# Optimization experiments

Hardware: AMD Instinct MI355X
Metric: run time of the kernel (lower is better)

The kernel has to match this reference:

```python
import jax, jax.numpy as jnp
import numpy as np

N_NODES = 100000


def _gcn_conv(x, src, dst, W, b):
    # symmetric normalization D^{-1/2} (A+I) D^{-1/2}, self loops already in src/dst
    deg = jax.ops.segment_sum(jnp.ones_like(src, dtype=x.dtype), dst, num_segments=N_NODES)
    dinv = jnp.where(deg > 0, jax.lax.rsqrt(jnp.maximum(deg, 1e-12)), 0.0)
    norm = dinv[src] * dinv[dst]                      # [E+N]
    h = x @ W                                          # [N, out] dense GEMM first (fewer features to move)
    msg = h[src] * norm[:, None]                       # gather + scale, [E+N, out]
    out = jax.ops.segment_sum(msg, dst, num_segments=N_NODES)
    return out + b


def setup_inputs() -> dict:
    key = jax.random.key(0)
    k_x, k_e, k_w1, k_w2 = jax.random.split(key, 4)
    in_f, hid, n_cls = 512, 128, 32
    E = 1600000
    x = jax.random.normal(k_x, (N_NODES, in_f), dtype=jnp.float32)
    edge_index = jax.random.randint(k_e, (2, E), 0, N_NODES, dtype=jnp.int32)
    # Glorot-ish init for weights
    W1 = jax.random.normal(k_w1, (in_f, hid), dtype=jnp.float32) * (1.0 / np.sqrt(in_f))
    b1 = jnp.zeros((hid,), dtype=jnp.float32)
    W2 = jax.random.normal(k_w2, (hid, n_cls), dtype=jnp.float32) * (1.0 / np.sqrt(hid))
    b2 = jnp.zeros((n_cls,), dtype=jnp.float32)
    return {"x": x, "edge_index": edge_index, "W1": W1, "b1": b1, "W2": W2, "b2": b2}


def reference(x, edge_index, W1, b1, W2, b2):
    loops = jnp.arange(N_NODES, dtype=edge_index.dtype)
    src = jnp.concatenate([edge_index[0], loops])
    dst = jnp.concatenate([edge_index[1], loops])
    h = _gcn_conv(x, src, dst, W1, b1)
    h = jax.nn.relu(h)
    # dropout in eval mode (identity) for deterministic reference
    out = _gcn_conv(h, src, dst, W2, b2)
    return out
```

## Files before the change

kernel.cpp:

```cpp
#include <hip/hip_runtime.h>
#include <hip/hip_bf16.h>
#include <cstddef>


#define IN_F 512
#define HID 128
#define NCLS 32

typedef __attribute__((ext_vector_type(8))) short bf16x8;
typedef __attribute__((ext_vector_type(4))) float f32x4;

__device__ __forceinline__ unsigned short f2bf(float f) {
    union { float f; unsigned u; } v; v.f = f;
    unsigned r = v.u + 0x7fff + ((v.u >> 16) & 1);
    return (unsigned short)(r >> 16);
}
__device__ __forceinline__ float bf2f(unsigned short h) {
    union { unsigned u; float f; } v; v.u = ((unsigned)h) << 16;
    return v.f;
}
__device__ __forceinline__ float lo16(unsigned u) { return bf2f((unsigned short)(u & 0xffff)); }
__device__ __forceinline__ float hi16(unsigned u) { return bf2f((unsigned short)(u >> 16)); }
__device__ __forceinline__ unsigned cvt_pk_bf16(float a, float b) {
    unsigned r;
    asm("v_cvt_pk_bf16_f32 %0, %1, %2" : "=v"(r) : "v"(a), "v"(b));
    return r;
}
__device__ __forceinline__ bf16x8 pk8(float4 lo, float4 hi) {
    union { uint4 u; bf16x8 v; } r;
    r.u.x = cvt_pk_bf16(lo.x, lo.y);
    r.u.y = cvt_pk_bf16(lo.z, lo.w);
    r.u.z = cvt_pk_bf16(hi.x, hi.y);
    r.u.w = cvt_pk_bf16(hi.z, hi.w);
    return r.v;
}

__global__ void k_histprep(const int* __restrict__ dst, int* __restrict__ deg,
                           int* __restrict__ rank, int E,
                           const float* __restrict__ W1, unsigned short* __restrict__ W1T,
                           const float* __restrict__ W2, unsigned short* __restrict__ W2T, int PB) {
    int b = blockIdx.x;
    if (b < PB) {
        int i = b * 256 + threadIdx.x;
        if (i < HID * IN_F) {
            int n = i >> 9, k = i & 511;
            W1T[(size_t)n * IN_F + k] = f2bf(W1[(size_t)k * HID + n]);
        } else {
            int j = i - HID * IN_F;
            int c = j >> 7, k = j & 127;
            W2T[(size_t)c * HID + k] = f2bf(W2[(size_t)k * NCLS + c]);
        }
    } else {
        int e = (b - PB) * 256 + threadIdx.x;
        if (e < E) rank[e] = atomicAdd(&deg[dst[e]], 1);
    }
}

__global__ __launch_bounds__(256) void k_scan1(const int* __restrict__ deg, int* __restrict__ rs,
                                               int* __restrict__ bsum, int n) {
    __shared__ int sd[256];
    int base = blockIdx.x * 2048 + threadIdx.x * 8;
    int v[8];
    int t = 0;
#pragma unroll
    for (int i = 0; i < 8; ++i) {
        int x = (base + i < n) ? ((deg[base + i] + 7) & ~7) : 0;
        v[i] = t;
        t += x;
    }
    sd[threadIdx.x] = t;
    __syncthreads();
    for (int off = 1; off < 256; off <<= 1) {
        int x = 0;
        if ((int)threadIdx.x >= off) x = sd[threadIdx.x - off];
        __syncthreads();
        if ((int)threadIdx.x >= off) sd[threadIdx.x] += x;
        __syncthreads();
    }
    int texcl = sd[threadIdx.x] - t;
#pragma unroll
    for (int i = 0; i < 8; ++i)
        if (base + i < n) rs[base + i] = texcl + v[i];
    if (threadIdx.x == 255) bsum[blockIdx.x] = sd[255];
}

__global__ __launch_bounds__(256) void k_scan3(int* __restrict__ rs, const int* __restrict__ bsum,
                                               const int* __restrict__ deg, int* __restrict__ csr,
                                               float* __restrict__ dinv,
                                               unsigned* __restrict__ hsu, unsigned* __restrict__ h2su,
                                               int n, int nb) {
    __shared__ int sb[256];
    __shared__ int se[256];
    int t = threadIdx.x;
    int val = (t < nb) ? bsum[t] : 0;
    sb[t] = val;
    __syncthreads();
    for (int off = 1; off < 256; off <<= 1) {
        int x = 0;
        if (t >= off) x = sb[t - off];
        __syncthreads();
        sb[t] += x;
        __syncthreads();
    }
    se[t] = sb[t] - val;
    __syncthreads();
    int i = blockIdx.x * 256 + t;
    if (i < n) {
        int d = deg[i];
        dinv[i] = rsqrtf((float)d + 1.0f);
        int r = rs[i] + se[i >> 11];
        rs[i] = r;
        int pc = (d + 7) & ~7;
        for (int j = d; j < pc; ++j) csr[r + j] = n;
    }
    if (blockIdx.x == 0) {
        if (t < 64) hsu[(size_t)n * 64 + t] = 0u;
        if (t < 16) h2su[(size_t)n * 16 + t] = 0u;
    }
}

#define SCHUNK 1024
__global__ __launch_bounds__(256) void k_fused(const float* __restrict__ A,
                                               const unsigned short* __restrict__ BT,
                                               const float* __restrict__ dinv,
                                               unsigned short* __restrict__ C, int M,
                                               const int* __restrict__ src, const int* __restrict__ dst,
                                               const int* __restrict__ rank, const int* __restrict__ rs,
                                               int* __restrict__ csr, int E) {
    const int bid = blockIdx.x;
    const int tid = threadIdx.x;
    if (bid & 1) {
        int base = (bid >> 1) * SCHUNK + tid;
        int d[4], s[4], rk[4];
        bool val[4];
#pragma unroll
        for (int j = 0; j < 4; ++j) {
            int e = base + j * 256;
            val[j] = e < E;
            if (val[j]) { d[j] = dst[e]; s[j] = src[e]; rk[j] = rank[e]; }
        }
#pragma unroll
        for (int j = 0; j < 4; ++j)
            if (val[j]) csr[rs[d[j]] + rk[j]] = s[j];
        return;
    }
    const int wave = tid >> 6;
    const int lane = tid & 63;
    const int l16 = lane & 15;
    const int q = lane >> 4;
    const int rowBase = (bid >> 1) * 64;
    const int arow = rowBase + wave * 16 + l16;
    const bool aval = arow < M;
    const float* aptr = A + (size_t)arow * IN_F + q * 8;
    const unsigned short* bptr = BT + (size_t)l16 * IN_F + q * 8;

    f32x4 acc[8];
#pragma unroll
    for (int nt = 0; nt < 8; ++nt) acc[nt] = (f32x4){0.f, 0.f, 0.f, 0.f};

    float4 a0, a1;
    bf16x8 bfr[8];
    auto ld = [&](int k0, float4& x0, float4& x1, bf16x8* bv) {
        if (aval) {
            x0 = *(const float4*)(aptr + k0);
            x1 = *(const float4*)(aptr + k0 + 4);
        } else {
            x0 = make_float4(0.f, 0.f, 0.f, 0.f);
            x1 = x0;
        }
#pragma unroll
        for (int nt = 0; nt < 8; ++nt)
            bv[nt] = *(const bf16x8*)(bptr + (size_t)nt * 16 * IN_F + k0);
    };

    ld(0, a0, a1, bfr);
    for (int t = 0; t < 16; ++t) {
        float4 na0, na1;
        bf16x8 nb[8];
        if (t < 15) ld((t + 1) * 32, na0, na1, nb);
        bf16x8 a_frag = pk8(a0, a1);
#pragma unroll
        for (int nt = 0; nt < 8; ++nt)
            acc[nt] = __builtin_amdgcn_mfma_f32_16x16x32_bf16(a_frag, bfr[nt], acc[nt], 0, 0, 0);
        a0 = na0; a1 = na1;
#pragma unroll
        for (int nt = 0; nt < 8; ++nt) bfr[nt] = nb[nt];
    }

#pragma unroll
    for (int r = 0; r < 4; ++r) {
        int row = rowBase + wave * 16 + q * 4 + r;
        if (row < M) {
            float sc = dinv[row];
#pragma unroll
            for (int nt = 0; nt < 8; ++nt)
                C[(size_t)row * HID + nt * 16 + l16] = f2bf(acc[nt][r] * sc);
        }
    }
}

__global__ __launch_bounds__(256) void k_agg1mm(const unsigned short* __restrict__ hs,
                                                const int* __restrict__ csr,
                                                const int* __restrict__ rs, const int* __restrict__ cnt,
                                                const float* __restrict__ dinv, const float* __restrict__ b1,
                                                const unsigned short* __restrict__ W2T,
                                                unsigned short* __restrict__ h2s, int N) {
    __shared__ unsigned h1s[16 * 68];
    const int tid = threadIdx.x;
    const int wave = tid >> 6;
    const int lane = tid & 63;
    const int base = blockIdx.x * 16;
    const unsigned* hrow = (const unsigned*)hs;
    float2 bb = ((const float2*)b1)[lane];
#pragma unroll
    for (int r = 0; r < 4; ++r) {
        int slot = wave * 4 + r;
        int v = base + slot;
        float ox = 0.f, oy = 0.f;
        if (v < N) {
            float dv = dinv[v];
            unsigned u = hrow[(size_t)v * 64 + lane];
            float ax = lo16(u), ay = hi16(u);
            int start = rs[v];
            int pc = (cnt[v] + 7) & ~7;
            for (int i = 0; i < pc; i += 8) {
                int s[8];
                unsigned uu[8];
#pragma unroll
                for (int j = 0; j < 8; ++j) s[j] = csr[start + i + j];
#pragma unroll
                for (int j = 0; j < 8; ++j) uu[j] = hrow[(size_t)s[j] * 64 + lane];
#pragma unroll
                for (int j = 0; j < 8; ++j) { ax += lo16(uu[j]); ay += hi16(uu[j]); }
            }
            ox = fmaxf(dv * ax + bb.x, 0.f);
            oy = fmaxf(dv * ay + bb.y, 0.f);
        }
        h1s[slot * 68 + lane] = cvt_pk_bf16(ox, oy);
    }
    __syncthreads();
    if (wave < 2) {
        const int l16 = lane & 15;
        const int q = lane >> 4;
        f32x4 acc = (f32x4){0.f, 0.f, 0.f, 0.f};
        const unsigned short* h1b = (const unsigned short*)h1s;
#pragma unroll
        for (int ks = 0; ks < 4; ++ks) {
            bf16x8 af = *(const bf16x8*)(h1b + l16 * 136 + ks * 32 + q * 8);
            bf16x8 bf_ = *(const bf16x8*)(W2T + (size_t)(wave * 16 + l16) * HID + ks * 32 + q * 8);
            acc = __builtin_amdgcn_mfma_f32_16x16x32_bf16(af, bf_, acc, 0, 0, 0);
        }
#pragma unroll
        for (int r = 0; r < 4; ++r) {
            int v = base + q * 4 + r;
            if (v < N)
                h2s[(size_t)v * NCLS + wave * 16 + l16] = f2bf(acc[r] * dinv[v]);
        }
    }
}

__global__ __launch_bounds__(256) void k_agg2(const unsigned short* __restrict__ h2s,
                                              const int* __restrict__ csr,
                                              const int* __restrict__ rs, const int* __restrict__ cnt,
                                              const float* __restrict__ dinv, const float* __restrict__ b2,
                                              float* __restrict__ out, int N) {
    int g = threadIdx.x >> 4;
    int l = threadIdx.x & 15;
    int v = blockIdx.x * 16 + g;
    if (v >= N) return;
    float dv = dinv[v];
    const unsigned* rows = (const unsigned*)h2s;
    unsigned u = rows[(size_t)v * 16 + l];
    float ax = lo16(u), ay = hi16(u);
    int start = rs[v];
    int pc = (cnt[v] + 7) & ~7;
    for (int i = 0; i < pc; i += 8) {
        int s[8];
        unsigned uu[8];
#pragma unroll
        for (int j = 0; j < 8; ++j) s[j] = csr[start + i + j];
#pragma unroll
        for (int j = 0; j < 8; ++j) uu[j] = rows[(size_t)s[j] * 16 + l];
#pragma unroll
        for (int j = 0; j < 8; ++j) { ax += lo16(uu[j]); ay += hi16(uu[j]); }
    }
    float2 bb = ((const float2*)b2)[l];
    float2 o;
    o.x = dv * ax + bb.x;
    o.y = dv * ay + bb.y;
    *((float2*)(out + (size_t)v * NCLS) + l) = o;
}

extern "C" void kernel_launch(void* const* d_in, const int* in_sizes, int n_in,
                              void* d_out, int out_size, void* d_ws, size_t ws_size,
                              hipStream_t stream) {
    const float* x = (const float*)d_in[0];
    const int* edge_index = (const int*)d_in[1];
    const float* W1 = (const float*)d_in[2];
    const float* b1 = (const float*)d_in[3];
    const float* W2 = (const float*)d_in[4];
    const float* b2 = (const float*)d_in[5];
    float* out = (float*)d_out;

    const int N = in_sizes[0] / IN_F;
    const int E = in_sizes[1] / 2;
    const int* e_src = edge_index;
    const int* e_dst = edge_index + E;

    char* ws = (char*)d_ws;
    size_t off = 0;
    auto alloc = [&](size_t bytes) -> char* {
        char* p = ws + off;
        off += (bytes + 255) & ~(size_t)255;
        return p;
    };
    int* deg             = (int*)alloc((size_t)N * 4);
    float* dinv          = (float*)alloc((size_t)N * 4);
    int* rs              = (int*)alloc((size_t)N * 4);
    int* bsum            = (int*)alloc(1024 * 4);
    int* csr             = (int*)alloc(((size_t)E + 8 * (size_t)N) * 4);
    unsigned short* W1T  = (unsigned short*)alloc((size_t)HID * IN_F * 2);
    unsigned short* W2T  = (unsigned short*)alloc((size_t)NCLS * HID * 2);
    unsigned short* hs   = (unsigned short*)alloc((size_t)(N + 1) * HID * 2);
    unsigned short* h2s  = (unsigned short*)alloc((size_t)(N + 1) * NCLS * 2);
    int* rank            = (int*)alloc((size_t)E * 4);

    const int nbE = (E + 255) / 256;
    const int nbN = (N + 255) / 256;
    const int nbScan = (N + 2047) / 2048;
    const int PB = (HID * IN_F + NCLS * HID) / 256;
    const int NBG = (N + 63) / 64;

    hipMemsetAsync(deg, 0, (size_t)N * 4, stream);
    k_histprep<<<PB + nbE, 256, 0, stream>>>(e_dst, deg, rank, E, W1, W1T, W2, W2T, PB);
    k_scan1<<<nbScan, 256, 0, stream>>>(deg, rs, bsum, N);
    k_scan3<<<nbN, 256, 0, stream>>>(rs, bsum, deg, csr, dinv, (unsigned*)hs, (unsigned*)h2s, N, nbScan);

    k_fused<<<2 * NBG, 256, 0, stream>>>(x, W1T, dinv, hs, N, e_src, e_dst, rank, rs, csr, E);

    k_agg1mm<<<(N + 15) / 16, 256, 0, stream>>>(hs, csr, rs, deg, dinv, b1, W2T, h2s, N);
    k_agg2<<<(N + 15) / 16, 256, 0, stream>>>(h2s, csr, rs, deg, dinv, b2, out, N);
}
```

Baseline: 649.8 us.

## Stage weight tiles in double-buffered LDS for the fused GEMM

The GEMM half of the fused kernel no longer has every wave load the full 128-column bf16 weight slice from global memory. The block loads each k-slice once, cooperatively, into two padded LDS buffers and reads the MFMA B fragments from there. It ping-pongs between the buffers with barriers so global prefetch overlaps the MFMAs. This cuts redundant global/L2 weight traffic (4x per block) but adds barriers, manual waitcnt synchronisation and LDS usage that may lower occupancy.

New measurement: 534.2 us. 1.22x faster.

```diff
diff --git a/kernel.cpp b/kernel.cpp
--- a/kernel.cpp
+++ b/kernel.cpp
@@ -119,6 +119,7 @@
     }
 }
 
+#define LSTR 40
 #define SCHUNK 1024
 __global__ __launch_bounds__(256) void k_fused(const float* __restrict__ A,
                                                const unsigned short* __restrict__ BT,
@@ -144,47 +145,108 @@
             if (val[j]) csr[rs[d[j]] + rk[j]] = s[j];
         return;
     }
+    __shared__ unsigned short Bs0[128 * LSTR];
+    __shared__ unsigned short Bs1[128 * LSTR];
     const int wave = tid >> 6;
     const int lane = tid & 63;
     const int l16 = lane & 15;
     const int q = lane >> 4;
     const int rowBase = (bid >> 1) * 64;
+
     const int arow = rowBase + wave * 16 + l16;
     const bool aval = arow < M;
     const float* aptr = A + (size_t)arow * IN_F + q * 8;
-    const unsigned short* bptr = BT + (size_t)l16 * IN_F + q * 8;
+
+    const int bn0 = tid >> 2, bn1 = 64 + (tid >> 2), bkc = tid & 3;
+    const unsigned short* bp0 = BT + (size_t)bn0 * IN_F + bkc * 8;
+    const unsigned short* bp1 = BT + (size_t)bn1 * IN_F + bkc * 8;
+    unsigned short* w0 = Bs0 + bn0 * LSTR + bkc * 8;
+    unsigned short* w1 = Bs0 + bn1 * LSTR + bkc * 8;
+    unsigned short* w2 = Bs1 + bn0 * LSTR + bkc * 8;
+    unsigned short* w3 = Bs1 + bn1 * LSTR + bkc * 8;
 
     f32x4 acc[8];
 #pragma unroll
     for (int nt = 0; nt < 8; ++nt) acc[nt] = (f32x4){0.f, 0.f, 0.f, 0.f};
 
-    float4 a0, a1;
-    bf16x8 bfr[8];
-    auto ld = [&](int k0, float4& x0, float4& x1, bf16x8* bv) {
-        if (aval) {
-            x0 = *(const float4*)(aptr + k0);
-            x1 = *(const float4*)(aptr + k0 + 4);
-        } else {
-            x0 = make_float4(0.f, 0.f, 0.f, 0.f);
-            x1 = x0;
-        }
-#pragma unroll
-        for (int nt = 0; nt < 8; ++nt)
-            bv[nt] = *(const bf16x8*)(bptr + (size_t)nt * 16 * IN_F + k0);
-    };
-
-    ld(0, a0, a1, bfr);
-    for (int t = 0; t < 16; ++t) {
-        float4 na0, na1;
-        bf16x8 nb[8];
-        if (t < 15) ld((t + 1) * 32, na0, na1, nb);
-        bf16x8 a_frag = pk8(a0, a1);
-#pragma unroll
-        for (int nt = 0; nt < 8; ++nt)
-            acc[nt] = __builtin_amdgcn_mfma_f32_16x16x32_bf16(a_frag, bfr[nt], acc[nt], 0, 0, 0);
-        a0 = na0; a1 = na1;
-#pragma unroll
-        for (int nt = 0; nt < 8; ++nt) bfr[nt] = nb[nt];
+    float4 zf = make_float4(0.f, 0.f, 0.f, 0.f);
+    float4 a0lo = zf, a0hi = zf, a1lo = zf, a1hi = zf;
+    uint4 b0a, b0b, b1a, b1b;
+
+    b0a = *(const uint4*)(bp0);
+    b0b = *(const uint4*)(bp1);
+    if (aval) { a0lo = *(const float4*)(aptr); a0hi = *(const float4*)(aptr + 4); }
+    *(uint4*)w0 = b0a;
+    *(uint4*)w1 = b0b;
+    b1a = *(const uint4*)(bp0 + 32);
+    b1b = *(const uint4*)(bp1 + 32);
+    if (aval) { a1lo = *(const float4*)(aptr + 32); a1hi = *(const float4*)(aptr + 36); }
+    asm volatile("s_waitcnt lgkmcnt(0)" ::: "memory");
+    __builtin_amdgcn_s_barrier();
+
+#pragma unroll 1
+    for (int tt = 0; tt < 8; ++tt) {
+        const int k = tt * 64;
+        *(uint4*)w2 = b1a;
+        *(uint4*)w3 = b1b;
+        {
+            bf16x8 a_frag = pk8(a0lo, a0hi);
+            if (tt < 7) {
+                b0a = *(const uint4*)(bp0 + k + 64);
+                b0b = *(const uint4*)(bp1 + k + 64);
+                if (aval) { a0lo = *(const float4*)(aptr + k + 64); a0hi = *(const float4*)(aptr + k + 68); }
+            }
+            bf16x8 bf0 = *(const bf16x8*)(Bs0 + (0 * 16 + l16) * LSTR + q * 8);
+            bf16x8 bf1 = *(const bf16x8*)(Bs0 + (1 * 16 + l16) * LSTR + q * 8);
+            bf16x8 bf2 = *(const bf16x8*)(Bs0 + (2 * 16 + l16) * LSTR + q * 8);
+            bf16x8 bf3 = *(const bf16x8*)(Bs0 + (3 * 16 + l16) * LSTR + q * 8);
+            bf16x8 bf4 = *(const bf16x8*)(Bs0 + (4 * 16 + l16) * LSTR + q * 8);
+            bf16x8 bf5 = *(const bf16x8*)(Bs0 + (5 * 16 + l16) * LSTR + q * 8);
+            bf16x8 bf6 = *(const bf16x8*)(Bs0 + (6 * 16 + l16) * LSTR + q * 8);
+            bf16x8 bf7 = *(const bf16x8*)(Bs0 + (7 * 16 + l16) * LSTR + q * 8);
+            acc[0] = __builtin_amdgcn_mfma_f32_16x16x32_bf16(a_frag, bf0, acc[0], 0, 0, 0);
+            acc[1] = __builtin_amdgcn_mfma_f32_16x16x32_bf16(a_frag, bf1, acc[1], 0, 0, 0);
+            acc[2] = __builtin_amdgcn_mfma_f32_16x16x32_bf16(a_frag, bf2, acc[2], 0, 0, 0);
+            acc[3] = __builtin_amdgcn_mfma_f32_16x16x32_bf16(a_frag, bf3, acc[3], 0, 0, 0);
+            acc[4] = __builtin_amdgcn_mfma_f32_16x16x32_bf16(a_frag, bf4, acc[4], 0, 0, 0);
+            acc[5] = __builtin_amdgcn_mfma_f32_16x16x32_bf16(a_frag, bf5, acc[5], 0, 0, 0);
+            acc[6] = __builtin_amdgcn_mfma_f32_16x16x32_bf16(a_frag, bf6, acc[6], 0, 0, 0);
+            acc[7] = __builtin_amdgcn_mfma_f32_16x16x32_bf16(a_frag, bf7, acc[7], 0, 0, 0);
+        }
+        asm volatile("s_waitcnt lgkmcnt(0)" ::: "memory");
+        __builtin_amdgcn_s_barrier();
+        if (tt < 7) {
+            *(uint4*)w0 = b0a;
+            *(uint4*)w1 = b0b;
+        }
+        {
+            bf16x8 a_frag = pk8(a1lo, a1hi);
+            if (tt < 7) {
+                b1a = *(const uint4*)(bp0 + k + 96);
+                b1b = *(const uint4*)(bp1 + k + 96);
+                if (aval) { a1lo = *(const float4*)(aptr + k + 96); a1hi = *(const float4*)(aptr + k + 100); }
+            }
+            bf16x8 bf0 = *(const bf16x8*)(Bs1 + (0 * 16 + l16) * LSTR + q * 8);
+            bf16x8 bf1 = *(const bf16x8*)(Bs1 + (1 * 16 + l16) * LSTR + q * 8);
+            bf16x8 bf2 = *(const bf16x8*)(Bs1 + (2 * 16 + l16) * LSTR + q * 8);
+            bf16x8 bf3 = *(const bf16x8*)(Bs1 + (3 * 16 + l16) * LSTR + q * 8);
+            bf16x8 bf4 = *(const bf16x8*)(Bs1 + (4 * 16 + l16) * LSTR + q * 8);
+            bf16x8 bf5 = *(const bf16x8*)(Bs1 + (5 * 16 + l16) * LSTR + q * 8);
+            bf16x8 bf6 = *(const bf16x8*)(Bs1 + (6 * 16 + l16) * LSTR + q * 8);
+            bf16x8 bf7 = *(const bf16x8*)(Bs1 + (7 * 16 + l16) * LSTR + q * 8);
+            acc[0] = __builtin_amdgcn_mfma_f32_16x16x32_bf16(a_frag, bf0, acc[0], 0, 0, 0);
+            acc[1] = __builtin_amdgcn_mfma_f32_16x16x32_bf16(a_frag, bf1, acc[1], 0, 0, 0);
+            acc[2] = __builtin_amdgcn_mfma_f32_16x16x32_bf16(a_frag, bf2, acc[2], 0, 0, 0);
+            acc[3] = __builtin_amdgcn_mfma_f32_16x16x32_bf16(a_frag, bf3, acc[3], 0, 0, 0);
+            acc[4] = __builtin_amdgcn_mfma_f32_16x16x32_bf16(a_frag, bf4, acc[4], 0, 0, 0);
+            acc[5] = __builtin_amdgcn_mfma_f32_16x16x32_bf16(a_frag, bf5, acc[5], 0, 0, 0);
+            acc[6] = __builtin_amdgcn_mfma_f32_16x16x32_bf16(a_frag, bf6, acc[6], 0, 0, 0);
+            acc[7] = __builtin_amdgcn_mfma_f32_16x16x32_bf16(a_frag, bf7, acc[7], 0, 0, 0);
+        }
+        if (tt < 7) {
+            asm volatile("s_waitcnt lgkmcnt(0)" ::: "memory");
+            __builtin_amdgcn_s_barrier();
+        }
     }
 
 #pragma unroll
```
